# Optimization experiments

Hardware: AMD Instinct MI355X
Metric: run time of the kernel (lower is better)

## Reference

```python
import jax, jax.numpy as jnp
import numpy as np

B, S, D = 16, 2048, 128

def setup_inputs() -> dict:
    key = jax.random.key(0)
    kq, kk, kv = jax.random.split(key, 3)
    queries = jax.random.normal(kq, (B, S, D), dtype=jnp.float32)
    keys = jax.random.normal(kk, (B, S, D), dtype=jnp.float32)
    values = jax.random.normal(kv, (B, S, D), dtype=jnp.float32)
    return {"queries": queries, "keys": keys, "values": values}

def reference(queries, keys, values):
    # scores: [B, S, S] = Q @ K^T / sqrt(D)
    d = queries.shape[-1]
    scores = jnp.einsum('bqd,bkd->bqk', queries, keys) / jnp.float32(np.sqrt(d))
    attn = jax.nn.softmax(scores, axis=-1)
    # dropout_rate=0.0 -> identity
    out = jnp.einsum('bqk,bkd->bqd', attn, values)
    return out
```

## Files before the change

### kernel.cpp

```cpp
#include <hip/hip_runtime.h>
#include <hip/hip_bf16.h>

#define BATCH 16
#define SEQ   2048
#define DIM   128
#define KTILE 64
#define NIT   (SEQ / KTILE)
#define QT    128
#define SCALE 0.08838834764831845f

typedef __bf16 bf16_t;
typedef __bf16 bf16x8 __attribute__((ext_vector_type(8)));
typedef __bf16 bf16x4 __attribute__((ext_vector_type(4)));
typedef float  f32x4  __attribute__((ext_vector_type(4)));

#define KSTR 136

__device__ __forceinline__ int rho(int s) {
    return (s & 32) | ((s & 4) << 2) | (((s >> 3) & 3) << 2) | (s & 3);
}
__device__ __forceinline__ int swz(int row) {
    return (row & 7) ^ ((row >> 2) & 7);
}

__global__ __launch_bounds__(512, 2)
void attn_fwd(const float* __restrict__ Qg, const float* __restrict__ Kg,
              const float* __restrict__ Vg, float* __restrict__ Og)
{
    __shared__ __align__(16) bf16_t sK [2][KTILE][KSTR];
    __shared__ __align__(16) bf16_t sVt[2][DIM][64];

    const int tid  = threadIdx.x;
    const int wave = tid >> 6;
    const int lane = tid & 63;
    const int l16  = lane & 15;
    const int g    = lane >> 4;

    const int bid   = blockIdx.x;
    const int batch = ((bid & 7) << 1) | ((bid >> 7) & 1);
    const int qtile = (bid >> 3) & 15;
    const int q0    = qtile * QT + wave * 16;

    const float* Kb = Kg + (size_t)batch * SEQ * DIM;
    const float* Vb = Vg + (size_t)batch * SEQ * DIM;

    bf16x8 qf[4];
    {
        const float* qp = Qg + ((size_t)batch * SEQ + q0 + l16) * DIM + g * 8;
        #pragma unroll
        for (int c = 0; c < 4; ++c) {
            const float4 u = *reinterpret_cast<const float4*>(qp + c * 32);
            const float4 v = *reinterpret_cast<const float4*>(qp + c * 32 + 4);
            bf16x8 f;
            f[0] = (bf16_t)(u.x * SCALE); f[1] = (bf16_t)(u.y * SCALE);
            f[2] = (bf16_t)(u.z * SCALE); f[3] = (bf16_t)(u.w * SCALE);
            f[4] = (bf16_t)(v.x * SCALE); f[5] = (bf16_t)(v.y * SCALE);
            f[6] = (bf16_t)(v.z * SCALE); f[7] = (bf16_t)(v.w * SCALE);
            qf[c] = f;
        }
    }

    const int krow = tid >> 3;
    const int kch  = tid & 7;
    const int vkg  = tid >> 5;
    const int vd4  = tid & 31;

    float4 ka[2][2];
    float4 va[4];

    auto load_tile = [&](int k0) {
        #pragma unroll
        for (int i = 0; i < 2; ++i) {
            const float* p = Kb + (size_t)(k0 + krow) * DIM + kch * 8 + i * 64;
            ka[i][0] = *reinterpret_cast<const float4*>(p);
            ka[i][1] = *reinterpret_cast<const float4*>(p + 4);
        }
        #pragma unroll
        for (int j = 0; j < 4; ++j)
            va[j] = *reinterpret_cast<const float4*>(
                Vb + (size_t)(k0 + vkg * 4 + j) * DIM + vd4 * 4);
    };
    auto write_tile = [&](int buf) {
        #pragma unroll
        for (int i = 0; i < 2; ++i) {
            const float* a = reinterpret_cast<const float*>(&ka[i][0]);
            bf16x8 w;
            #pragma unroll
            for (int e = 0; e < 8; ++e) w[e] = (bf16_t)a[e];
            *reinterpret_cast<bf16x8*>(&sK[buf][rho(krow)][kch * 8 + i * 64]) = w;
        }
        #pragma unroll
        for (int dd = 0; dd < 4; ++dd) {
            const int row = vd4 * 4 + dd;
            const int col = (((vkg >> 1) ^ swz(row)) << 3) + ((vkg & 1) << 2);
            bf16x4 w;
            w[0] = (bf16_t)va[0][dd]; w[1] = (bf16_t)va[1][dd];
            w[2] = (bf16_t)va[2][dd]; w[3] = (bf16_t)va[3][dd];
            *reinterpret_cast<bf16x4*>(&sVt[buf][row][col]) = w;
        }
    };

    const f32x4 vzero = {0.f, 0.f, 0.f, 0.f};
    f32x4 o[8];
    #pragma unroll
    for (int i = 0; i < 8; ++i) o[i] = vzero;
    float lsum = 0.f;

    load_tile(0);
    write_tile(0);
    load_tile(KTILE);

    for (int it = 0; it < NIT; ++it) {
        __syncthreads();

        if (it + 1 < NIT) {
            write_tile((it + 1) & 1);
            if (it + 2 < NIT) load_tile((it + 2) * KTILE);
        }
        const int cur = it & 1;

        f32x4 sc[4];
        #pragma unroll
        for (int ksb = 0; ksb < 4; ++ksb) sc[ksb] = vzero;
        #pragma unroll
        for (int c = 0; c < 4; ++c) {
            #pragma unroll
            for (int ksb = 0; ksb < 4; ++ksb) {
                bf16x8 kf = *reinterpret_cast<const bf16x8*>(
                    &sK[cur][ksb * 16 + l16][c * 32 + g * 8]);
                sc[ksb] = __builtin_amdgcn_mfma_f32_16x16x32_bf16(
                    kf, qf[c], sc[ksb], 0, 0, 0);
            }
        }

        float pe[16];
        #pragma unroll
        for (int ksb = 0; ksb < 4; ++ksb) {
            #pragma unroll
            for (int r = 0; r < 4; ++r) {
                const float p = __expf(sc[ksb][r]);
                pe[ksb * 4 + r] = p;
                lsum += p;
            }
        }
        bf16x8 pb[2];
        #pragma unroll
        for (int c2 = 0; c2 < 2; ++c2) {
            bf16x8 t;
            #pragma unroll
            for (int jj = 0; jj < 8; ++jj)
                t[jj] = (bf16_t)pe[(2 * c2 + (jj >> 2)) * 4 + (jj & 3)];
            pb[c2] = t;
        }

        #pragma unroll
        for (int n0 = 0; n0 < 8; ++n0) {
            const int row = n0 * 16 + l16;
            #pragma unroll
            for (int c2 = 0; c2 < 2; ++c2) {
                bf16x8 vf = *reinterpret_cast<const bf16x8*>(
                    &sVt[cur][row][((c2 * 4 + g) ^ swz(row)) << 3]);
                o[n0] = __builtin_amdgcn_mfma_f32_16x16x32_bf16(
                    vf, pb[c2], o[n0], 0, 0, 0);
            }
        }
    }

    float l = lsum;
    l += __shfl_xor(l, 16);
    l += __shfl_xor(l, 32);
    const float inv = 1.f / l;
    float* op = Og + ((size_t)batch * SEQ + q0 + l16) * DIM + g * 4;
    #pragma unroll
    for (int n0 = 0; n0 < 8; ++n0) {
        float4 st = { o[n0][0] * inv, o[n0][1] * inv,
                      o[n0][2] * inv, o[n0][3] * inv };
        *reinterpret_cast<float4*>(op + n0 * 16) = st;
    }
}

extern "C" void kernel_launch(void* const* d_in, const int* in_sizes, int n_in,
                              void* d_out, int out_size, void* d_ws, size_t ws_size,
                              hipStream_t stream) {
    const float* Q = (const float*)d_in[0];
    const float* K = (const float*)d_in[1];
    const float* V = (const float*)d_in[2];
    float* O = (float*)d_out;
    dim3 grid(BATCH * SEQ / QT);
    dim3 block(512);
    hipLaunchKernelGGL(attn_fwd, grid, block, 0, stream, Q, K, V, O);
}
```

Baseline: 135.5 us.

## Specialize waves into producer loaders and consumers computing two query sub-tiles

Splits the 8 waves into 4 loader waves that fetch K/V from global memory, convert to bf16 and write shared memory, and 4 compute waves that each handle 32 query rows (two 16-row sub-tiles). Each K/V fragment read from LDS now feeds two MFMAs, which halves LDS reads per query row, and the global-load latency is moved off the compute waves. The cost is that only half the waves issue MFMAs, compute waves hold twice the accumulator and Q registers, and loader waves idle at the barrier, so occupancy and register pressure may become the limit.

```diff
diff --git a/kernel.cpp b/kernel.cpp
--- a/kernel.cpp
+++ b/kernel.cpp
@@ -35,122 +35,153 @@
     const int lane = tid & 63;
     const int l16  = lane & 15;
     const int g    = lane >> 4;
+    const bool is_comp = (wave < 4);
 
     const int bid   = blockIdx.x;
     const int batch = ((bid & 7) << 1) | ((bid >> 7) & 1);
     const int qtile = (bid >> 3) & 15;
-    const int q0    = qtile * QT + wave * 16;
+    const int q0    = qtile * QT + wave * 32;
 
     const float* Kb = Kg + (size_t)batch * SEQ * DIM;
     const float* Vb = Vg + (size_t)batch * SEQ * DIM;
 
-    bf16x8 qf[4];
-    {
-        const float* qp = Qg + ((size_t)batch * SEQ + q0 + l16) * DIM + g * 8;
-        #pragma unroll
-        for (int c = 0; c < 4; ++c) {
-            const float4 u = *reinterpret_cast<const float4*>(qp + c * 32);
-            const float4 v = *reinterpret_cast<const float4*>(qp + c * 32 + 4);
-            bf16x8 f;
-            f[0] = (bf16_t)(u.x * SCALE); f[1] = (bf16_t)(u.y * SCALE);
-            f[2] = (bf16_t)(u.z * SCALE); f[3] = (bf16_t)(u.w * SCALE);
-            f[4] = (bf16_t)(v.x * SCALE); f[5] = (bf16_t)(v.y * SCALE);
-            f[6] = (bf16_t)(v.z * SCALE); f[7] = (bf16_t)(v.w * SCALE);
-            qf[c] = f;
-        }
-    }
-
-    const int krow = tid >> 3;
-    const int kch  = tid & 7;
-    const int vkg  = tid >> 5;
-    const int vd4  = tid & 31;
-
-    float4 ka[2][2];
-    float4 va[4];
+    bf16x8 qf[2][4];
+    if (is_comp) {
+        #pragma unroll
+        for (int h = 0; h < 2; ++h) {
+            const float* qp =
+                Qg + ((size_t)batch * SEQ + q0 + h * 16 + l16) * DIM + g * 8;
+            #pragma unroll
+            for (int c = 0; c < 4; ++c) {
+                const float4 u = *reinterpret_cast<const float4*>(qp + c * 32);
+                const float4 v = *reinterpret_cast<const float4*>(qp + c * 32 + 4);
+                bf16x8 f;
+                f[0] = (bf16_t)(u.x * SCALE); f[1] = (bf16_t)(u.y * SCALE);
+                f[2] = (bf16_t)(u.z * SCALE); f[3] = (bf16_t)(u.w * SCALE);
+                f[4] = (bf16_t)(v.x * SCALE); f[5] = (bf16_t)(v.y * SCALE);
+                f[6] = (bf16_t)(v.z * SCALE); f[7] = (bf16_t)(v.w * SCALE);
+                qf[h][c] = f;
+            }
+        }
+    }
+
+    const int p    = tid & 255;
+    const int krow = p >> 3;
+    const int kch  = p & 7;
+    const int vkg  = p >> 5;
+    const int vd4  = p & 31;
+
+    float4 ka[2][2][2];
+    float4 va[2][4];
 
     auto load_tile = [&](int k0) {
         #pragma unroll
-        for (int i = 0; i < 2; ++i) {
-            const float* p = Kb + (size_t)(k0 + krow) * DIM + kch * 8 + i * 64;
-            ka[i][0] = *reinterpret_cast<const float4*>(p);
-            ka[i][1] = *reinterpret_cast<const float4*>(p + 4);
-        }
-        #pragma unroll
-        for (int j = 0; j < 4; ++j)
-            va[j] = *reinterpret_cast<const float4*>(
-                Vb + (size_t)(k0 + vkg * 4 + j) * DIM + vd4 * 4);
+        for (int r = 0; r < 2; ++r) {
+            #pragma unroll
+            for (int i = 0; i < 2; ++i) {
+                const float* pp =
+                    Kb + (size_t)(k0 + krow + r * 32) * DIM + kch * 8 + i * 64;
+                ka[r][i][0] = *reinterpret_cast<const float4*>(pp);
+                ka[r][i][1] = *reinterpret_cast<const float4*>(pp + 4);
+            }
+            #pragma unroll
+            for (int j = 0; j < 4; ++j)
+                va[r][j] = *reinterpret_cast<const float4*>(
+                    Vb + (size_t)(k0 + (vkg + r * 8) * 4 + j) * DIM + vd4 * 4);
+        }
     };
     auto write_tile = [&](int buf) {
         #pragma unroll
-        for (int i = 0; i < 2; ++i) {
-            const float* a = reinterpret_cast<const float*>(&ka[i][0]);
-            bf16x8 w;
-            #pragma unroll
-            for (int e = 0; e < 8; ++e) w[e] = (bf16_t)a[e];
-            *reinterpret_cast<bf16x8*>(&sK[buf][rho(krow)][kch * 8 + i * 64]) = w;
-        }
-        #pragma unroll
-        for (int dd = 0; dd < 4; ++dd) {
-            const int row = vd4 * 4 + dd;
-            const int col = (((vkg >> 1) ^ swz(row)) << 3) + ((vkg & 1) << 2);
-            bf16x4 w;
-            w[0] = (bf16_t)va[0][dd]; w[1] = (bf16_t)va[1][dd];
-            w[2] = (bf16_t)va[2][dd]; w[3] = (bf16_t)va[3][dd];
-            *reinterpret_cast<bf16x4*>(&sVt[buf][row][col]) = w;
+        for (int r = 0; r < 2; ++r) {
+            const int row = krow + r * 32;
+            #pragma unroll
+            for (int i = 0; i < 2; ++i) {
+                const float* a = reinterpret_cast<const float*>(&ka[r][i][0]);
+                bf16x8 w;
+                #pragma unroll
+                for (int e = 0; e < 8; ++e) w[e] = (bf16_t)a[e];
+                *reinterpret_cast<bf16x8*>(&sK[buf][rho(row)][kch * 8 + i * 64]) = w;
+            }
+            const int kg = vkg + r * 8;
+            #pragma unroll
+            for (int dd = 0; dd < 4; ++dd) {
+                const int vrow = vd4 * 4 + dd;
+                const int col = (((kg >> 1) ^ swz(vrow)) << 3) + ((kg & 1) << 2);
+                bf16x4 w;
+                w[0] = (bf16_t)va[r][0][dd]; w[1] = (bf16_t)va[r][1][dd];
+                w[2] = (bf16_t)va[r][2][dd]; w[3] = (bf16_t)va[r][3][dd];
+                *reinterpret_cast<bf16x4*>(&sVt[buf][vrow][col]) = w;
+            }
         }
     };
 
     const f32x4 vzero = {0.f, 0.f, 0.f, 0.f};
-    f32x4 o[8];
+    f32x4 o[2][8];
     #pragma unroll
-    for (int i = 0; i < 8; ++i) o[i] = vzero;
-    float lsum = 0.f;
-
-    load_tile(0);
-    write_tile(0);
-    load_tile(KTILE);
+    for (int h = 0; h < 2; ++h)
+        #pragma unroll
+        for (int i = 0; i < 8; ++i) o[h][i] = vzero;
+    float lsum[2] = {0.f, 0.f};
+
+    if (!is_comp) {
+        load_tile(0);
+        write_tile(0);
+        load_tile(KTILE);
+    }
 
     for (int it = 0; it < NIT; ++it) {
         __syncthreads();
 
-        if (it + 1 < NIT) {
-            write_tile((it + 1) & 1);
-            if (it + 2 < NIT) load_tile((it + 2) * KTILE);
-        }
+        if (!is_comp) {
+            if (it + 1 < NIT) {
+                write_tile((it + 1) & 1);
+                if (it + 2 < NIT) load_tile((it + 2) * KTILE);
+            }
+            continue;
+        }
+
         const int cur = it & 1;
 
-        f32x4 sc[4];
-        #pragma unroll
-        for (int ksb = 0; ksb < 4; ++ksb) sc[ksb] = vzero;
+        f32x4 sc[2][4];
+        #pragma unroll
+        for (int ksb = 0; ksb < 4; ++ksb) { sc[0][ksb] = vzero; sc[1][ksb] = vzero; }
         #pragma unroll
         for (int c = 0; c < 4; ++c) {
             #pragma unroll
             for (int ksb = 0; ksb < 4; ++ksb) {
                 bf16x8 kf = *reinterpret_cast<const bf16x8*>(
                     &sK[cur][ksb * 16 + l16][c * 32 + g * 8]);
-                sc[ksb] = __builtin_amdgcn_mfma_f32_16x16x32_bf16(
-                    kf, qf[c], sc[ksb], 0, 0, 0);
-            }
-        }
-
-        float pe[16];
-        #pragma unroll
-        for (int ksb = 0; ksb < 4; ++ksb) {
-            #pragma unroll
-            for (int r = 0; r < 4; ++r) {
-                const float p = __expf(sc[ksb][r]);
-                pe[ksb * 4 + r] = p;
-                lsum += p;
-            }
-        }
-        bf16x8 pb[2];
-        #pragma unroll
-        for (int c2 = 0; c2 < 2; ++c2) {
-            bf16x8 t;
-            #pragma unroll
-            for (int jj = 0; jj < 8; ++jj)
-                t[jj] = (bf16_t)pe[(2 * c2 + (jj >> 2)) * 4 + (jj & 3)];
-            pb[c2] = t;
+                sc[0][ksb] = __builtin_amdgcn_mfma_f32_16x16x32_bf16(
+                    kf, qf[0][c], sc[0][ksb], 0, 0, 0);
+                sc[1][ksb] = __builtin_amdgcn_mfma_f32_16x16x32_bf16(
+                    kf, qf[1][c], sc[1][ksb], 0, 0, 0);
+            }
+        }
+
+        float pe[2][16];
+        #pragma unroll
+        for (int h = 0; h < 2; ++h) {
+            #pragma unroll
+            for (int ksb = 0; ksb < 4; ++ksb) {
+                #pragma unroll
+                for (int r = 0; r < 4; ++r) {
+                    const float pv = __expf(sc[h][ksb][r]);
+                    pe[h][ksb * 4 + r] = pv;
+                    lsum[h] += pv;
+                }
+            }
+        }
+        bf16x8 pb[2][2];
+        #pragma unroll
+        for (int h = 0; h < 2; ++h) {
+            #pragma unroll
+            for (int c2 = 0; c2 < 2; ++c2) {
+                bf16x8 t;
+                #pragma unroll
+                for (int jj = 0; jj < 8; ++jj)
+                    t[jj] = (bf16_t)pe[h][(2 * c2 + (jj >> 2)) * 4 + (jj & 3)];
+                pb[h][c2] = t;
+            }
         }
 
         #pragma unroll
@@ -160,22 +191,29 @@
             for (int c2 = 0; c2 < 2; ++c2) {
                 bf16x8 vf = *reinterpret_cast<const bf16x8*>(
                     &sVt[cur][row][((c2 * 4 + g) ^ swz(row)) << 3]);
-                o[n0] = __builtin_amdgcn_mfma_f32_16x16x32_bf16(
-                    vf, pb[c2], o[n0], 0, 0, 0);
-            }
-        }
-    }
-
-    float l = lsum;
-    l += __shfl_xor(l, 16);
-    l += __shfl_xor(l, 32);
-    const float inv = 1.f / l;
-    float* op = Og + ((size_t)batch * SEQ + q0 + l16) * DIM + g * 4;
-    #pragma unroll
-    for (int n0 = 0; n0 < 8; ++n0) {
-        float4 st = { o[n0][0] * inv, o[n0][1] * inv,
-                      o[n0][2] * inv, o[n0][3] * inv };
-        *reinterpret_cast<float4*>(op + n0 * 16) = st;
+                o[0][n0] = __builtin_amdgcn_mfma_f32_16x16x32_bf16(
+                    vf, pb[0][c2], o[0][n0], 0, 0, 0);
+                o[1][n0] = __builtin_amdgcn_mfma_f32_16x16x32_bf16(
+                    vf, pb[1][c2], o[1][n0], 0, 0, 0);
+            }
+        }
+    }
+
+    if (is_comp) {
+        #pragma unroll
+        for (int h = 0; h < 2; ++h) {
+            float l = lsum[h];
+            l += __shfl_xor(l, 16);
+            l += __shfl_xor(l, 32);
+            const float inv = 1.f / l;
+            float* op = Og + ((size_t)batch * SEQ + q0 + h * 16 + l16) * DIM + g * 4;
+            #pragma unroll
+            for (int n0 = 0; n0 < 8; ++n0) {
+                float4 st = { o[h][n0][0] * inv, o[h][n0][1] * inv,
+                              o[h][n0][2] * inv, o[h][n0][3] * inv };
+                *reinterpret_cast<float4*>(op + n0 * 16) = st;
+            }
+        }
     }
 }
 
```

Measured after the change: 127.8 us. 1.06x faster.
